# Kernel optimization log

Measured on AMD Instinct MI355X. Metric: run time of the kernel, lower is better.

The kernel has to match this reference:

```python
import jax, jax.numpy as jnp
import numpy as np

B, T, D, H = 8, 2048, 1024, 128  # batch, seq, input_size, head_size


def setup_inputs() -> dict:
    key = jax.random.key(0)
    kx, kq, kk, kv = jax.random.split(key, 4)
    s = 1.0 / np.sqrt(D)
    return {
        "x": jax.random.normal(kx, (B, T, D), dtype=jnp.float32),
        "Wq": jax.random.normal(kq, (D, H), dtype=jnp.float32) * s,
        "Wk": jax.random.normal(kk, (D, H), dtype=jnp.float32) * s,
        "Wv": jax.random.normal(kv, (D, H), dtype=jnp.float32) * s,
    }


def reference(x, Wq, Wk, Wv):
    # projections (Linear, no bias)
    q = jnp.einsum("btd,dh->bth", x, Wq)
    k = jnp.einsum("btd,dh->bth", x, Wk)
    v = jnp.einsum("btd,dh->bth", x, Wv)
    scale = H ** (-0.5)
    scores = jnp.einsum("bth,bsh->bts", q, k) * scale  # [B,T,T]
    t = x.shape[1]
    causal = jnp.tril(jnp.ones((t, t), dtype=bool))
    scores = jnp.where(causal, scores, -jnp.inf)
    attn = jax.nn.softmax(scores, axis=-1)  # dropout p=0.0 -> identity
    out = jnp.einsum("bts,bsh->bth", attn, v)
    return out
```

## Files before the change

kernel.cpp:

```cpp
#include <hip/hip_runtime.h>
#include <math.h>

#define B_ 8
#define T_ 2048
#define D_ 1024
#define H_ 128
#define BT (B_ * T_)

typedef short bf16x8 __attribute__((ext_vector_type(8)));
typedef float f32x4 __attribute__((ext_vector_type(4)));

static constexpr float SCALE = 0.08838834764831845f;

__device__ inline unsigned short f2b(float f) {
  unsigned int u = __float_as_uint(f);
  u += 0x7FFF + ((u >> 16) & 1);
  return (unsigned short)(u >> 16);
}
__device__ inline unsigned int pk2(float a, float b) {
  return (unsigned int)f2b(a) | ((unsigned int)f2b(b) << 16);
}

__device__ __forceinline__ void gll16(const void* g, void* l) {
  __builtin_amdgcn_global_load_lds(
      (const __attribute__((address_space(1))) void*)g,
      (__attribute__((address_space(3))) void*)l, 16, 0, 0);
}

__global__ __launch_bounds__(256) void wcvt_kernel(
    const float* __restrict__ Wq, const float* __restrict__ Wk,
    const float* __restrict__ Wv, short* __restrict__ Wt) {
  __shared__ short Wls[128 * 72];
  const int sel = blockIdx.y;
  const float* W = sel == 0 ? Wq : (sel == 1 ? Wk : Wv);
  const int d0 = blockIdx.x * 64;
  const int tid = threadIdx.x;
#pragma unroll
  for (int i = 0; i < 8; ++i) {
    int slot = tid + i * 256;
    int r = slot >> 5, hg = slot & 31;
    float4 w = *(const float4*)(W + (size_t)(d0 + r) * H_ + hg * 4);
    Wls[(hg * 4 + 0) * 72 + r] = (short)f2b(w.x);
    Wls[(hg * 4 + 1) * 72 + r] = (short)f2b(w.y);
    Wls[(hg * 4 + 2) * 72 + r] = (short)f2b(w.z);
    Wls[(hg * 4 + 3) * 72 + r] = (short)f2b(w.w);
  }
  __syncthreads();
  short* dst = Wt + (size_t)sel * D_ * H_;
#pragma unroll
  for (int i = 0; i < 4; ++i) {
    int slot = tid + i * 256;
    int h = slot >> 3, g = slot & 7;
    *(int4*)(dst + (size_t)h * D_ + d0 + g * 8) = *(int4*)&Wls[h * 72 + g * 8];
  }
}

__global__ __launch_bounds__(256) void proj_kernel(
    const float* __restrict__ x, const short* __restrict__ Wt,
    short* __restrict__ qb, short* __restrict__ kb, short* __restrict__ vtb) {
  __shared__ alignas(16) char smem[49152];
  short* Xs0 = (short*)smem;
  short* Xs1 = (short*)(smem + 8192);
  short* Ws0 = (short*)(smem + 16384);
  short* Ws1 = (short*)(smem + 32768);

  const int tid = threadIdx.x;
  const int wave = tid >> 6, lane = tid & 63;
  const int ln = lane & 15, quad = lane >> 4;
  const int mw = wave & 1, nw = wave >> 1;
  const int sel = blockIdx.y;
  const int row0 = blockIdx.x * 64;
  const short* W = Wt + (size_t)sel * (size_t)(D_ * H_);

  f32x4 acc[2][4];
#pragma unroll
  for (int mi = 0; mi < 2; ++mi)
#pragma unroll
    for (int ni = 0; ni < 4; ++ni) acc[mi][ni] = (f32x4){0.f, 0.f, 0.f, 0.f};

  auto stage = [&](int bf, int k0) {
    short* Ws = bf ? Ws1 : Ws0;
#pragma unroll
    for (int j = 0; j < 4; ++j) {
      const int rbase = wave * 32 + j * 8;
      const int n = rbase + (lane >> 3);
      const int gp = (lane & 7) ^ (n & 7);
      gll16(W + (size_t)n * D_ + k0 + gp * 8, (char*)Ws + rbase * 128);
    }
    short* Xs = bf ? Xs1 : Xs0;
    float4 xr[4];
#pragma unroll
    for (int i = 0; i < 4; ++i) {
      int fid = tid + i * 256;
      int r = fid >> 4, g4 = fid & 15;
      xr[i] = *(const float4*)(x + (size_t)(row0 + r) * D_ + k0 + g4 * 4);
    }
#pragma unroll
    for (int i = 0; i < 4; ++i) {
      int fid = tid + i * 256;
      int r = fid >> 4, g4 = fid & 15;
      int g = g4 >> 1, half = g4 & 1;
      unsigned int* p = (unsigned int*)&Xs[r * 64 + ((g ^ (r & 7)) * 8) + half * 4];
      p[0] = pk2(xr[i].x, xr[i].y);
      p[1] = pk2(xr[i].z, xr[i].w);
    }
  };

  stage(0, 0);
  for (int s = 0; s < 16; ++s) {
    __syncthreads();
    if (s < 15) stage((s + 1) & 1, (s + 1) * 64);
    const short* Xs = (s & 1) ? Xs1 : Xs0;
    const short* Ws = (s & 1) ? Ws1 : Ws0;
#pragma unroll
    for (int kk = 0; kk < 2; ++kk) {
      bf16x8 a[2];
#pragma unroll
      for (int mi = 0; mi < 2; ++mi) {
        int r = mw * 32 + mi * 16 + ln;
        a[mi] = *(bf16x8*)&Xs[r * 64 + (((kk * 4 + quad) ^ (r & 7)) * 8)];
      }
#pragma unroll
      for (int ni = 0; ni < 4; ++ni) {
        int n = nw * 64 + ni * 16 + ln;
        bf16x8 bb = *(bf16x8*)&Ws[n * 64 + (((kk * 4 + quad) ^ (n & 7)) * 8)];
#pragma unroll
        for (int mi = 0; mi < 2; ++mi)
          acc[mi][ni] = __builtin_amdgcn_mfma_f32_16x16x32_bf16(a[mi], bb, acc[mi][ni], 0, 0, 0);
      }
    }
  }

  __syncthreads();
  short* Cs = (short*)smem;
  if (sel < 2) {
    short* out = sel ? kb : qb;
#pragma unroll
    for (int mi = 0; mi < 2; ++mi)
#pragma unroll
      for (int ni = 0; ni < 4; ++ni)
#pragma unroll
        for (int rr = 0; rr < 4; ++rr)
          Cs[(mw * 32 + mi * 16 + quad * 4 + rr) * 136 + nw * 64 + ni * 16 + ln] =
              (short)f2b(acc[mi][ni][rr]);
    __syncthreads();
#pragma unroll
    for (int i = 0; i < 4; ++i) {
      int slot = tid + i * 256;
      int r = slot >> 4, g = slot & 15;
      *(int4*)(out + (size_t)(row0 + r) * H_ + g * 8) = *(int4*)&Cs[r * 136 + g * 8];
    }
  } else {
#pragma unroll
    for (int mi = 0; mi < 2; ++mi)
#pragma unroll
      for (int ni = 0; ni < 4; ++ni)
#pragma unroll
        for (int rr = 0; rr < 4; ++rr)
          Cs[(nw * 64 + ni * 16 + ln) * 72 + mw * 32 + mi * 16 + quad * 4 + rr] =
              (short)f2b(acc[mi][ni][rr]);
    __syncthreads();
    const int b = row0 >> 11, t0 = row0 & 2047;
#pragma unroll
    for (int i = 0; i < 4; ++i) {
      int slot = tid + i * 256;
      int h = slot >> 3, g = slot & 7;
      *(int4*)(vtb + (size_t)(b * H_ + h) * T_ + t0 + g * 8) = *(int4*)&Cs[h * 72 + g * 8];
    }
  }
}

__global__ __launch_bounds__(128) void attn_kernel(
    const short* __restrict__ qb, const short* __restrict__ kb,
    const short* __restrict__ vtb, float* __restrict__ out) {
  __shared__ alignas(16) char smem[69888];
  short* Ks0 = (short*)smem;
  short* Ks1 = (short*)(smem + 16384);
  short* Vt0 = (short*)(smem + 32768);
  short* Vt1 = (short*)(smem + 49152);
  short* Pt  = (short*)(smem + 65536);

  const int tid = threadIdx.x;
  const int wv = tid >> 6, lane = tid & 63;
  const int ln = lane & 15, quad = lane >> 4;
  const int slot = blockIdx.x & 255;
  const int pass = blockIdx.x >> 8;
  const int b = slot >> 5;
  const int j = slot & 31;
  const int tile = pass ? (63 - j) : j;
  const int q0 = tile * 32;

  short* myP = Pt + wv * (16 * 68);

  bf16x8 qfr[4];
#pragma unroll
  for (int kk = 0; kk < 4; ++kk)
    qfr[kk] = *(const bf16x8*)(qb + (size_t)(b * T_ + q0 + wv * 16 + ln) * H_ +
                               kk * 32 + quad * 8);

  f32x4 oacc[8];
#pragma unroll
  for (int ht = 0; ht < 8; ++ht) oacc[ht] = (f32x4){0.f, 0.f, 0.f, 0.f};

  float m_run = -INFINITY, l_run = 0.f;
  const int qglob = q0 + wv * 16 + ln;

  auto stageK = [&](short* dst, int s0) {
#pragma unroll
    for (int jj = 0; jj < 8; ++jj) {
      const int rb = wv * 32 + jj * 4;
      const int r = rb + (lane >> 4);
      const int gp = (lane & 15) ^ (r & 7);
      gll16(kb + (size_t)(b * T_ + s0 + r) * H_ + gp * 8, (char*)dst + rb * 256);
    }
  };
  auto stageV = [&](short* dst, int s0) {
#pragma unroll
    for (int jj = 0; jj < 8; ++jj) {
      const int hb = wv * 64 + jj * 8;
      const int h = hb + (lane >> 3);
      const int gp = (lane & 7) ^ (h & 7);
      gll16(vtb + (size_t)(b * H_ + h) * T_ + s0 + gp * 8, (char*)dst + hb * 128);
    }
  };

  const int nch = (q0 >> 6) + 1;
  stageK(Ks0, 0);
  stageV(Vt0, 0);

  for (int ch = 0; ch < nch; ++ch) {
    const int s0 = ch * 64;
    const int cur = ch & 1;
    __syncthreads();
    if (ch + 1 < nch) {
      stageK(cur ? Ks0 : Ks1, s0 + 64);
      stageV(cur ? Vt0 : Vt1, s0 + 64);
    }
    const short* Kc = cur ? Ks1 : Ks0;
    const short* Vc = cur ? Vt1 : Vt0;

    f32x4 sacc[4];
#pragma unroll
    for (int t = 0; t < 4; ++t) sacc[t] = (f32x4){0.f, 0.f, 0.f, 0.f};
#pragma unroll
    for (int kk = 0; kk < 4; ++kk) {
#pragma unroll
      for (int t = 0; t < 4; ++t) {
        const int krow = t * 16 + ln;
        bf16x8 kf = *(bf16x8*)&Kc[krow * 128 + (((kk * 4 + quad) ^ (ln & 7)) * 8)];
        sacc[t] = __builtin_amdgcn_mfma_f32_16x16x32_bf16(kf, qfr[kk], sacc[t], 0, 0, 0);
      }
    }

    float sv[4][4];
    float mc = -INFINITY;
#pragma unroll
    for (int t = 0; t < 4; ++t)
#pragma unroll
      for (int r = 0; r < 4; ++r) {
        const int key = s0 + t * 16 + quad * 4 + r;
        float s = sacc[t][r] * SCALE;
        sv[t][r] = (key <= qglob) ? s : -INFINITY;
        mc = fmaxf(mc, sv[t][r]);
      }
    mc = fmaxf(mc, __shfl_xor(mc, 16));
    mc = fmaxf(mc, __shfl_xor(mc, 32));
    const float mnew = fmaxf(m_run, mc);
    const float alpha = __expf(m_run - mnew);
    float lc = 0.f;
    float p[4][4];
#pragma unroll
    for (int t = 0; t < 4; ++t)
#pragma unroll
      for (int r = 0; r < 4; ++r) {
        p[t][r] = __expf(sv[t][r] - mnew);
        lc += p[t][r];
      }
    lc += __shfl_xor(lc, 16);
    lc += __shfl_xor(lc, 32);
    l_run = l_run * alpha + lc;
    m_run = mnew;

#pragma unroll
    for (int t = 0; t < 4; ++t) {
      *(unsigned int*)&myP[ln * 68 + t * 16 + quad * 4 + 0] = pk2(p[t][0], p[t][1]);
      *(unsigned int*)&myP[ln * 68 + t * 16 + quad * 4 + 2] = pk2(p[t][2], p[t][3]);
    }
#pragma unroll
    for (int ht = 0; ht < 8; ++ht)
#pragma unroll
      for (int r = 0; r < 4; ++r) oacc[ht][r] *= alpha;

#pragma unroll
    for (int kk2 = 0; kk2 < 2; ++kk2) {
      bf16x8 pf = *(bf16x8*)&myP[ln * 68 + kk2 * 32 + quad * 8];
#pragma unroll
      for (int ht = 0; ht < 8; ++ht) {
        const int hrow = ht * 16 + ln;
        bf16x8 vf = *(bf16x8*)&Vc[hrow * 64 + (((kk2 * 4 + quad) ^ (ln & 7)) * 8)];
        oacc[ht] = __builtin_amdgcn_mfma_f32_16x16x32_bf16(vf, pf, oacc[ht], 0, 0, 0);
      }
    }
  }

  const float linv = 1.0f / l_run;
#pragma unroll
  for (int ht = 0; ht < 8; ++ht)
#pragma unroll
    for (int r = 0; r < 4; ++r) oacc[ht][r] *= linv;

  __syncthreads();
  float* Ot = (float*)smem;
#pragma unroll
  for (int ht = 0; ht < 8; ++ht)
    *(f32x4*)&Ot[(wv * 16 + ln) * 132 + ht * 16 + quad * 4] = oacc[ht];
  __syncthreads();
#pragma unroll
  for (int i = 0; i < 8; ++i) {
    int slot2 = tid + i * 128;
    int r = slot2 >> 5, c = slot2 & 31;
    float4 v = *(float4*)&Ot[r * 132 + c * 4];
    *(float4*)(out + (size_t)(b * T_ + q0 + r) * H_ + c * 4) = v;
  }
}

extern "C" void kernel_launch(void* const* d_in, const int* in_sizes, int n_in,
                              void* d_out, int out_size, void* d_ws, size_t ws_size,
                              hipStream_t stream) {
  const float* x  = (const float*)d_in[0];
  const float* Wq = (const float*)d_in[1];
  const float* Wk = (const float*)d_in[2];
  const float* Wv = (const float*)d_in[3];
  float* out = (float*)d_out;

  char* ws = (char*)d_ws;
  short* qb  = (short*)(ws);
  short* kb  = (short*)(ws + 4194304);
  short* vtb = (short*)(ws + 8388608);
  short* Wt  = (short*)(ws + 12582912);

  wcvt_kernel<<<dim3(D_ / 64, 3), 256, 0, stream>>>(Wq, Wk, Wv, Wt);
  proj_kernel<<<dim3(BT / 64, 3), 256, 0, stream>>>(x, Wt, qb, kb, vtb);
  attn_kernel<<<dim3(512), 128, 0, stream>>>(qb, kb, vtb, out);
}
```

Before: 172.4 us.

## Split causal attention into key-segment partials with a separate combine kernel

The attention kernel becomes split-KV: each block handles a 64-query tile and a segment of up to 8 key chunks, using 4 waves of 256 threads. It writes unnormalized partial outputs plus running max and sum to workspace. A new reduce kernel merges the segments with log-sum-exp rescaling and normalizes. The goal is to balance the causal triangle across 640 roughly equal blocks, at the cost of an extra launch and partial-output traffic through global memory.

```diff
diff --git a/kernel.cpp b/kernel.cpp
--- a/kernel.cpp
+++ b/kernel.cpp
@@ -170,10 +170,11 @@
   }
 }
 
-__global__ __launch_bounds__(128) void attn_kernel(
+__global__ __launch_bounds__(256) void attn_part(
     const short* __restrict__ qb, const short* __restrict__ kb,
-    const short* __restrict__ vtb, float* __restrict__ out) {
-  __shared__ alignas(16) char smem[69888];
+    const short* __restrict__ vtb, float* __restrict__ po,
+    float* __restrict__ pm, float* __restrict__ pl) {
+  __shared__ alignas(16) char smem[74240];
   short* Ks0 = (short*)smem;
   short* Ks1 = (short*)(smem + 16384);
   short* Vt0 = (short*)(smem + 32768);
@@ -183,12 +184,15 @@
   const int tid = threadIdx.x;
   const int wv = tid >> 6, lane = tid & 63;
   const int ln = lane & 15, quad = lane >> 4;
-  const int slot = blockIdx.x & 255;
-  const int pass = blockIdx.x >> 8;
-  const int b = slot >> 5;
-  const int j = slot & 31;
-  const int tile = pass ? (63 - j) : j;
-  const int q0 = tile * 32;
+  const int b = blockIdx.x / 80;
+  const int rr = 79 - (blockIdx.x % 80);
+  const int g = (rr >= 48) ? 3 : (rr >= 24) ? 2 : (rr >= 8) ? 1 : 0;
+  const int local = rr - 4 * g * (g + 1);
+  const int j = 8 * g + local / (g + 1);
+  const int s = local - (local / (g + 1)) * (g + 1);
+  const int sid = b * 80 + rr;
+  const int q0 = j * 64;
+  const int nchunks = min(8, j + 1 - 8 * s);
 
   short* myP = Pt + wv * (16 * 68);
 
@@ -207,8 +211,8 @@
 
   auto stageK = [&](short* dst, int s0) {
 #pragma unroll
-    for (int jj = 0; jj < 8; ++jj) {
-      const int rb = wv * 32 + jj * 4;
+    for (int jj = 0; jj < 4; ++jj) {
+      const int rb = wv * 16 + jj * 4;
       const int r = rb + (lane >> 4);
       const int gp = (lane & 15) ^ (r & 7);
       gll16(kb + (size_t)(b * T_ + s0 + r) * H_ + gp * 8, (char*)dst + rb * 256);
@@ -216,23 +220,22 @@
   };
   auto stageV = [&](short* dst, int s0) {
 #pragma unroll
-    for (int jj = 0; jj < 8; ++jj) {
-      const int hb = wv * 64 + jj * 8;
+    for (int jj = 0; jj < 4; ++jj) {
+      const int hb = wv * 32 + jj * 8;
       const int h = hb + (lane >> 3);
       const int gp = (lane & 7) ^ (h & 7);
       gll16(vtb + (size_t)(b * H_ + h) * T_ + s0 + gp * 8, (char*)dst + hb * 128);
     }
   };
 
-  const int nch = (q0 >> 6) + 1;
-  stageK(Ks0, 0);
-  stageV(Vt0, 0);
-
-  for (int ch = 0; ch < nch; ++ch) {
-    const int s0 = ch * 64;
+  stageK(Ks0, 8 * s * 64);
+  stageV(Vt0, 8 * s * 64);
+
+  for (int ch = 0; ch < nchunks; ++ch) {
+    const int s0 = (8 * s + ch) * 64;
     const int cur = ch & 1;
     __syncthreads();
-    if (ch + 1 < nch) {
+    if (ch + 1 < nchunks) {
       stageK(cur ? Ks0 : Ks1, s0 + 64);
       stageV(cur ? Vt0 : Vt1, s0 + 64);
     }
@@ -259,8 +262,8 @@
 #pragma unroll
       for (int r = 0; r < 4; ++r) {
         const int key = s0 + t * 16 + quad * 4 + r;
-        float s = sacc[t][r] * SCALE;
-        sv[t][r] = (key <= qglob) ? s : -INFINITY;
+        float sc = sacc[t][r] * SCALE;
+        sv[t][r] = (key <= qglob) ? sc : -INFINITY;
         mc = fmaxf(mc, sv[t][r]);
       }
     mc = fmaxf(mc, __shfl_xor(mc, 16));
@@ -303,24 +306,69 @@
     }
   }
 
-  const float linv = 1.0f / l_run;
-#pragma unroll
-  for (int ht = 0; ht < 8; ++ht)
-#pragma unroll
-    for (int r = 0; r < 4; ++r) oacc[ht][r] *= linv;
-
+  if (quad == 0) {
+    pm[(size_t)sid * 64 + wv * 16 + ln] = m_run;
+    pl[(size_t)sid * 64 + wv * 16 + ln] = l_run;
+  }
   __syncthreads();
   float* Ot = (float*)smem;
 #pragma unroll
   for (int ht = 0; ht < 8; ++ht)
     *(f32x4*)&Ot[(wv * 16 + ln) * 132 + ht * 16 + quad * 4] = oacc[ht];
   __syncthreads();
+  float* dst = po + (size_t)sid * 8192;
 #pragma unroll
   for (int i = 0; i < 8; ++i) {
-    int slot2 = tid + i * 128;
-    int r = slot2 >> 5, c = slot2 & 31;
-    float4 v = *(float4*)&Ot[r * 132 + c * 4];
-    *(float4*)(out + (size_t)(b * T_ + q0 + r) * H_ + c * 4) = v;
+    int slot2 = tid + i * 256;
+    int r2 = slot2 >> 5, c2 = slot2 & 31;
+    *(f32x4*)(dst + r2 * 128 + c2 * 4) = *(f32x4*)&Ot[r2 * 132 + c2 * 4];
+  }
+}
+
+__global__ __launch_bounds__(256) void attn_reduce(
+    const float* __restrict__ po, const float* __restrict__ pm,
+    const float* __restrict__ pl, float* __restrict__ out) {
+  const int b = blockIdx.x >> 5;
+  const int j = blockIdx.x & 31;
+  const int g = j >> 3;
+  const int nseg = g + 1;
+  const int sid0 = b * 80 + 4 * g * (g + 1) + (j - 8 * g) * nseg;
+  const int tid = threadIdx.x;
+  const int q = tid >> 2, hq = tid & 3;
+
+  float m[4], l[4], a[4];
+  float M = -INFINITY;
+  for (int s2 = 0; s2 < nseg; ++s2) {
+    m[s2] = pm[(size_t)(sid0 + s2) * 64 + q];
+    l[s2] = pl[(size_t)(sid0 + s2) * 64 + q];
+    M = fmaxf(M, m[s2]);
+  }
+  float lsum = 0.f;
+  for (int s2 = 0; s2 < nseg; ++s2) {
+    a[s2] = __expf(m[s2] - M);
+    lsum += a[s2] * l[s2];
+  }
+  f32x4 acc[8];
+#pragma unroll
+  for (int i = 0; i < 8; ++i) acc[i] = (f32x4){0.f, 0.f, 0.f, 0.f};
+  for (int s2 = 0; s2 < nseg; ++s2) {
+    const float* src = po + (size_t)(sid0 + s2) * 8192 + q * 128 + hq * 32;
+    const float as = a[s2];
+#pragma unroll
+    for (int i = 0; i < 8; ++i) {
+      f32x4 v = *(const f32x4*)(src + i * 4);
+#pragma unroll
+      for (int c = 0; c < 4; ++c) acc[i][c] += as * v[c];
+    }
+  }
+  const float inv = 1.0f / lsum;
+  float* o = out + ((size_t)(b * T_ + j * 64 + q)) * H_ + hq * 32;
+#pragma unroll
+  for (int i = 0; i < 8; ++i) {
+    f32x4 v;
+#pragma unroll
+    for (int c = 0; c < 4; ++c) v[c] = acc[i][c] * inv;
+    *(f32x4*)(o + i * 4) = v;
   }
 }
 
@@ -338,8 +386,12 @@
   short* kb  = (short*)(ws + 4194304);
   short* vtb = (short*)(ws + 8388608);
   short* Wt  = (short*)(ws + 12582912);
+  float* po  = (float*)(ws + 14680064);
+  float* pm  = (float*)(ws + 35651584);
+  float* pl  = (float*)(ws + 35915776);
 
   wcvt_kernel<<<dim3(D_ / 64, 3), 256, 0, stream>>>(Wq, Wk, Wv, Wt);
   proj_kernel<<<dim3(BT / 64, 3), 256, 0, stream>>>(x, Wt, qb, kb, vtb);
-  attn_kernel<<<dim3(512), 128, 0, stream>>>(qb, kb, vtb, out);
-}
+  attn_part<<<dim3(8 * 80), 256, 0, stream>>>(qb, kb, vtb, po, pm, pl);
+  attn_reduce<<<dim3(8 * 32), 256, 0, stream>>>(po, pm, pl, out);
+}
```

Measured after the change: 165.7 us. 1.04x faster.

## Split causal attention into key-segment partials with a separate merge kernel

Applied to the files above, without the earlier changes.

Attention is restructured into a split-K scheme. Single-wave blocks each handle 16 queries over up to eight 64-key chunks, reading K and V fragments straight from global memory instead of double-buffered LDS, and write bf16 partial outputs plus running max and sum. A new reduce kernel merges the segments. The code also folds log2(e) into the scale so it can use exp2f, skips causal masking on chunks that lie fully below the diagonal, and in the projection kernel issues the next x loads before the MFMA loop and packs them afterward. This aims to balance the triangular workload across many more blocks, at the cost of an extra launch, partial-result traffic, bf16 rounding of partials, and uncoalesced global fragment loads.

```diff
diff --git a/kernel.cpp b/kernel.cpp
--- a/kernel.cpp
+++ b/kernel.cpp
@@ -10,7 +10,7 @@
 typedef short bf16x8 __attribute__((ext_vector_type(8)));
 typedef float f32x4 __attribute__((ext_vector_type(4)));
 
-static constexpr float SCALE = 0.08838834764831845f;
+static constexpr float SCALE2 = 0.127517416f;
 
 __device__ inline unsigned short f2b(float f) {
   unsigned int u = __float_as_uint(f);
@@ -19,6 +19,9 @@
 }
 __device__ inline unsigned int pk2(float a, float b) {
   return (unsigned int)f2b(a) | ((unsigned int)f2b(b) << 16);
+}
+__device__ inline float b2f(unsigned short u) {
+  return __uint_as_float((unsigned int)u << 16);
 }
 
 __device__ __forceinline__ void gll16(const void* g, void* l) {
@@ -78,7 +81,7 @@
 #pragma unroll
     for (int ni = 0; ni < 4; ++ni) acc[mi][ni] = (f32x4){0.f, 0.f, 0.f, 0.f};
 
-  auto stage = [&](int bf, int k0) {
+  auto stageW = [&](int bf, int k0) {
     short* Ws = bf ? Ws1 : Ws0;
 #pragma unroll
     for (int j = 0; j < 4; ++j) {
@@ -87,14 +90,9 @@
       const int gp = (lane & 7) ^ (n & 7);
       gll16(W + (size_t)n * D_ + k0 + gp * 8, (char*)Ws + rbase * 128);
     }
+  };
+  auto packX = [&](int bf, const float4* xr) {
     short* Xs = bf ? Xs1 : Xs0;
-    float4 xr[4];
-#pragma unroll
-    for (int i = 0; i < 4; ++i) {
-      int fid = tid + i * 256;
-      int r = fid >> 4, g4 = fid & 15;
-      xr[i] = *(const float4*)(x + (size_t)(row0 + r) * D_ + k0 + g4 * 4);
-    }
 #pragma unroll
     for (int i = 0; i < 4; ++i) {
       int fid = tid + i * 256;
@@ -106,10 +104,32 @@
     }
   };
 
-  stage(0, 0);
+  {
+    stageW(0, 0);
+    float4 xr[4];
+#pragma unroll
+    for (int i = 0; i < 4; ++i) {
+      int fid = tid + i * 256;
+      int r = fid >> 4, g4 = fid & 15;
+      xr[i] = *(const float4*)(x + (size_t)(row0 + r) * D_ + g4 * 4);
+    }
+    packX(0, xr);
+  }
+
   for (int s = 0; s < 16; ++s) {
     __syncthreads();
-    if (s < 15) stage((s + 1) & 1, (s + 1) * 64);
+    float4 xr[4];
+    const bool pre = (s < 15);
+    if (pre) {
+      const int k0n = (s + 1) * 64;
+      stageW((s + 1) & 1, k0n);
+#pragma unroll
+      for (int i = 0; i < 4; ++i) {
+        int fid = tid + i * 256;
+        int r = fid >> 4, g4 = fid & 15;
+        xr[i] = *(const float4*)(x + (size_t)(row0 + r) * D_ + k0n + g4 * 4);
+      }
+    }
     const short* Xs = (s & 1) ? Xs1 : Xs0;
     const short* Ws = (s & 1) ? Ws1 : Ws0;
 #pragma unroll
@@ -129,6 +149,7 @@
           acc[mi][ni] = __builtin_amdgcn_mfma_f32_16x16x32_bf16(a[mi], bb, acc[mi][ni], 0, 0, 0);
       }
     }
+    if (pre) packX((s + 1) & 1, xr);
   }
 
   __syncthreads();
@@ -170,32 +191,34 @@
   }
 }
 
-__global__ __launch_bounds__(128) void attn_kernel(
+__global__ __launch_bounds__(64, 3) void attn_part(
     const short* __restrict__ qb, const short* __restrict__ kb,
-    const short* __restrict__ vtb, float* __restrict__ out) {
-  __shared__ alignas(16) char smem[69888];
-  short* Ks0 = (short*)smem;
-  short* Ks1 = (short*)(smem + 16384);
-  short* Vt0 = (short*)(smem + 32768);
-  short* Vt1 = (short*)(smem + 49152);
-  short* Pt  = (short*)(smem + 65536);
-
-  const int tid = threadIdx.x;
-  const int wv = tid >> 6, lane = tid & 63;
+    const short* __restrict__ vtb, short* __restrict__ po,
+    float* __restrict__ pm, float* __restrict__ pl) {
+  __shared__ short myP[16 * 68];
+
+  const int lane = threadIdx.x;
   const int ln = lane & 15, quad = lane >> 4;
-  const int slot = blockIdx.x & 255;
-  const int pass = blockIdx.x >> 8;
-  const int b = slot >> 5;
-  const int j = slot & 31;
-  const int tile = pass ? (63 - j) : j;
-  const int q0 = tile * 32;
-
-  short* myP = Pt + wv * (16 * 68);
+  const int b = blockIdx.x & 7;
+  const int task = 319 - (blockIdx.x >> 3);
+  int a, base, nseg;
+  if (task < 32)       { a = task >> 2;              base = 4 * a;             nseg = 1; }
+  else if (task < 96)  { a = 8 + ((task - 32) >> 3); base = 32 + 8 * (a - 8);  nseg = 2; }
+  else if (task < 192) { a = 16 + (task - 96) / 12;  base = 96 + 12 * (a - 16); nseg = 3; }
+  else                 { a = 24 + ((task - 192) >> 4); base = 192 + 16 * (a - 24); nseg = 4; }
+  const int local = task - base;
+  const int ti = local / nseg;
+  const int s = local - ti * nseg;
+  const int j2 = 4 * a + ti;
+  const int q0 = j2 * 16;
+  const int c = a + 1;
+  const int ch0 = 8 * s, ch1 = min(8 * s + 8, c);
+  const int sid = b * 320 + task;
 
   bf16x8 qfr[4];
 #pragma unroll
   for (int kk = 0; kk < 4; ++kk)
-    qfr[kk] = *(const bf16x8*)(qb + (size_t)(b * T_ + q0 + wv * 16 + ln) * H_ +
+    qfr[kk] = *(const bf16x8*)(qb + (size_t)(b * T_ + q0 + ln) * H_ +
                                kk * 32 + quad * 8);
 
   f32x4 oacc[8];
@@ -203,41 +226,13 @@
   for (int ht = 0; ht < 8; ++ht) oacc[ht] = (f32x4){0.f, 0.f, 0.f, 0.f};
 
   float m_run = -INFINITY, l_run = 0.f;
-  const int qglob = q0 + wv * 16 + ln;
-
-  auto stageK = [&](short* dst, int s0) {
-#pragma unroll
-    for (int jj = 0; jj < 8; ++jj) {
-      const int rb = wv * 32 + jj * 4;
-      const int r = rb + (lane >> 4);
-      const int gp = (lane & 15) ^ (r & 7);
-      gll16(kb + (size_t)(b * T_ + s0 + r) * H_ + gp * 8, (char*)dst + rb * 256);
-    }
-  };
-  auto stageV = [&](short* dst, int s0) {
-#pragma unroll
-    for (int jj = 0; jj < 8; ++jj) {
-      const int hb = wv * 64 + jj * 8;
-      const int h = hb + (lane >> 3);
-      const int gp = (lane & 7) ^ (h & 7);
-      gll16(vtb + (size_t)(b * H_ + h) * T_ + s0 + gp * 8, (char*)dst + hb * 128);
-    }
-  };
-
-  const int nch = (q0 >> 6) + 1;
-  stageK(Ks0, 0);
-  stageV(Vt0, 0);
-
-  for (int ch = 0; ch < nch; ++ch) {
+  const int qg = q0 + ln;
+
+  const short* kbase = kb + (size_t)b * T_ * H_;
+  const short* vbase = vtb + (size_t)b * H_ * T_;
+
+  for (int ch = ch0; ch < ch1; ++ch) {
     const int s0 = ch * 64;
-    const int cur = ch & 1;
-    __syncthreads();
-    if (ch + 1 < nch) {
-      stageK(cur ? Ks0 : Ks1, s0 + 64);
-      stageV(cur ? Vt0 : Vt1, s0 + 64);
-    }
-    const short* Kc = cur ? Ks1 : Ks0;
-    const short* Vc = cur ? Vt1 : Vt0;
 
     f32x4 sacc[4];
 #pragma unroll
@@ -246,34 +241,38 @@
     for (int kk = 0; kk < 4; ++kk) {
 #pragma unroll
       for (int t = 0; t < 4; ++t) {
-        const int krow = t * 16 + ln;
-        bf16x8 kf = *(bf16x8*)&Kc[krow * 128 + (((kk * 4 + quad) ^ (ln & 7)) * 8)];
+        bf16x8 kf = *(const bf16x8*)(kbase + (size_t)(s0 + t * 16 + ln) * H_ +
+                                     kk * 32 + quad * 8);
         sacc[t] = __builtin_amdgcn_mfma_f32_16x16x32_bf16(kf, qfr[kk], sacc[t], 0, 0, 0);
       }
     }
 
+    const bool needMask = (s0 + 63 > q0);
     float sv[4][4];
     float mc = -INFINITY;
 #pragma unroll
     for (int t = 0; t < 4; ++t)
 #pragma unroll
       for (int r = 0; r < 4; ++r) {
-        const int key = s0 + t * 16 + quad * 4 + r;
-        float s = sacc[t][r] * SCALE;
-        sv[t][r] = (key <= qglob) ? s : -INFINITY;
-        mc = fmaxf(mc, sv[t][r]);
+        float scv = sacc[t][r] * SCALE2;
+        if (needMask) {
+          const int key = s0 + t * 16 + quad * 4 + r;
+          scv = (key <= qg) ? scv : -INFINITY;
+        }
+        sv[t][r] = scv;
+        mc = fmaxf(mc, scv);
       }
     mc = fmaxf(mc, __shfl_xor(mc, 16));
     mc = fmaxf(mc, __shfl_xor(mc, 32));
     const float mnew = fmaxf(m_run, mc);
-    const float alpha = __expf(m_run - mnew);
+    const float alpha = exp2f(m_run - mnew);
     float lc = 0.f;
     float p[4][4];
 #pragma unroll
     for (int t = 0; t < 4; ++t)
 #pragma unroll
       for (int r = 0; r < 4; ++r) {
-        p[t][r] = __expf(sv[t][r] - mnew);
+        p[t][r] = exp2f(sv[t][r] - mnew);
         lc += p[t][r];
       }
     lc += __shfl_xor(lc, 16);
@@ -296,32 +295,74 @@
       bf16x8 pf = *(bf16x8*)&myP[ln * 68 + kk2 * 32 + quad * 8];
 #pragma unroll
       for (int ht = 0; ht < 8; ++ht) {
-        const int hrow = ht * 16 + ln;
-        bf16x8 vf = *(bf16x8*)&Vc[hrow * 64 + (((kk2 * 4 + quad) ^ (ln & 7)) * 8)];
+        bf16x8 vf = *(const bf16x8*)(vbase + (size_t)(ht * 16 + ln) * T_ +
+                                     s0 + kk2 * 32 + quad * 8);
         oacc[ht] = __builtin_amdgcn_mfma_f32_16x16x32_bf16(vf, pf, oacc[ht], 0, 0, 0);
       }
     }
   }
 
-  const float linv = 1.0f / l_run;
-#pragma unroll
-  for (int ht = 0; ht < 8; ++ht)
-#pragma unroll
-    for (int r = 0; r < 4; ++r) oacc[ht][r] *= linv;
-
-  __syncthreads();
-  float* Ot = (float*)smem;
-#pragma unroll
-  for (int ht = 0; ht < 8; ++ht)
-    *(f32x4*)&Ot[(wv * 16 + ln) * 132 + ht * 16 + quad * 4] = oacc[ht];
-  __syncthreads();
-#pragma unroll
-  for (int i = 0; i < 8; ++i) {
-    int slot2 = tid + i * 128;
-    int r = slot2 >> 5, c = slot2 & 31;
-    float4 v = *(float4*)&Ot[r * 132 + c * 4];
-    *(float4*)(out + (size_t)(b * T_ + q0 + r) * H_ + c * 4) = v;
-  }
+  if (quad == 0) {
+    pm[(size_t)sid * 16 + ln] = m_run;
+    pl[(size_t)sid * 16 + ln] = l_run;
+  }
+  short* dst = po + (size_t)sid * 2048;
+#pragma unroll
+  for (int ht = 0; ht < 8; ++ht) {
+    int2 w2;
+    w2.x = (int)pk2(oacc[ht][0], oacc[ht][1]);
+    w2.y = (int)pk2(oacc[ht][2], oacc[ht][3]);
+    *(int2*)(dst + ln * 128 + ht * 16 + quad * 4) = w2;
+  }
+}
+
+__global__ __launch_bounds__(256) void attn_reduce(
+    const short* __restrict__ po, const float* __restrict__ pm,
+    const float* __restrict__ pl, float* __restrict__ out) {
+  const int b = blockIdx.x >> 7;
+  const int j2 = blockIdx.x & 127;
+  const int a = j2 >> 2;
+  const int nseg = (a >> 3) + 1;
+  const int base = (a < 8) ? 4 * a
+                 : (a < 16) ? 32 + 8 * (a - 8)
+                 : (a < 24) ? 96 + 12 * (a - 16)
+                 : 192 + 16 * (a - 24);
+  const int sid0 = b * 320 + base + (j2 & 3) * nseg;
+  const int tid = threadIdx.x;
+  const int q = tid >> 4, h0 = (tid & 15) * 8;
+
+  float m2[4], l[4], w[4];
+  float M2 = -INFINITY;
+  for (int s2 = 0; s2 < nseg; ++s2) {
+    m2[s2] = pm[(size_t)(sid0 + s2) * 16 + q];
+    l[s2] = pl[(size_t)(sid0 + s2) * 16 + q];
+    M2 = fmaxf(M2, m2[s2]);
+  }
+  float lsum = 0.f;
+  for (int s2 = 0; s2 < nseg; ++s2) {
+    w[s2] = exp2f(m2[s2] - M2);
+    lsum += w[s2] * l[s2];
+  }
+  float acc[8];
+#pragma unroll
+  for (int i = 0; i < 8; ++i) acc[i] = 0.f;
+  for (int s2 = 0; s2 < nseg; ++s2) {
+    int4 v = *(const int4*)(po + (size_t)(sid0 + s2) * 2048 + q * 128 + h0);
+    const unsigned int* pu = (const unsigned int*)&v;
+    const float as = w[s2];
+#pragma unroll
+    for (int cidx = 0; cidx < 4; ++cidx) {
+      unsigned int u = pu[cidx];
+      acc[cidx * 2 + 0] += as * b2f((unsigned short)(u & 0xFFFF));
+      acc[cidx * 2 + 1] += as * b2f((unsigned short)(u >> 16));
+    }
+  }
+  const float inv = 1.0f / lsum;
+  float* o = out + ((size_t)(b * T_ + j2 * 16 + q)) * H_ + h0;
+  float4 v0 = make_float4(acc[0] * inv, acc[1] * inv, acc[2] * inv, acc[3] * inv);
+  float4 v1 = make_float4(acc[4] * inv, acc[5] * inv, acc[6] * inv, acc[7] * inv);
+  *(float4*)(o + 0) = v0;
+  *(float4*)(o + 4) = v1;
 }
 
 extern "C" void kernel_launch(void* const* d_in, const int* in_sizes, int n_in,
@@ -338,8 +379,12 @@
   short* kb  = (short*)(ws + 4194304);
   short* vtb = (short*)(ws + 8388608);
   short* Wt  = (short*)(ws + 12582912);
+  short* po  = (short*)(ws + 14680064);
+  float* pm  = (float*)(ws + 25165824);
+  float* pl  = (float*)(ws + 25329664);
 
   wcvt_kernel<<<dim3(D_ / 64, 3), 256, 0, stream>>>(Wq, Wk, Wv, Wt);
   proj_kernel<<<dim3(BT / 64, 3), 256, 0, stream>>>(x, Wt, qb, kb, vtb);
-  attn_kernel<<<dim3(512), 128, 0, stream>>>(qb, kb, vtb, out);
-}
+  attn_part<<<dim3(2560), 64, 0, stream>>>(qb, kb, vtb, po, pm, pl);
+  attn_reduce<<<dim3(8 * 128), 256, 0, stream>>>(po, pm, pl, out);
+}
```

Measured after the change: 201.0 us. 16.6% more time.
